# Kernel optimization log

Hardware: AMD Instinct MI355X
Metric: run time of the kernel (lower is better)

## Reference

```python
import jax, jax.numpy as jnp
import numpy as np
import itertools

N = 65536          # points
R = 1.0 / 16.0     # radius (forward uses 1/16)
K = 64             # max_num_neighbors in forward call
G = 16             # grid cells per axis (cell size == R)


def _radius_knn_edges(pts):
    """Grid-hashed radius search; per point keep nearest K within R (self-loop included),
    pad with self index so every point has exactly K edges (max-aggregation neutral)."""
    cells = np.minimum((pts / R).astype(np.int64), G - 1)
    cid = (cells[:, 0] * G + cells[:, 1]) * G + cells[:, 2]
    order = np.argsort(cid, kind='stable')
    sorted_cid = cid[order]
    counts = np.bincount(cid, minlength=G ** 3)
    starts = np.concatenate([[0], np.cumsum(counts)[:-1]])
    M = int(counts.max())
    cand = -np.ones((G ** 3, M), dtype=np.int64)
    slot = np.arange(N) - starts[sorted_cid]
    cand[sorted_cid, slot] = order
    offs = np.array(list(itertools.product([-1, 0, 1], repeat=3)))
    nbr = np.empty((N, K), dtype=np.int64)
    chunk = 4096
    for s in range(0, N, chunk):
        e = min(s + chunk, N)
        c = cells[s:e]
        nc = c[:, None, :] + offs[None]                      # [B,27,3]
        valid_c = np.all((nc >= 0) & (nc < G), axis=-1)      # [B,27]
        ncid = (nc[..., 0] * G + nc[..., 1]) * G + nc[..., 2]
        ncid = np.where(valid_c, ncid, 0)
        cd = cand[ncid]                                      # [B,27,M]
        cd = np.where(np.broadcast_to(valid_c[..., None], cd.shape), cd, -1)
        cd = cd.reshape(e - s, -1)                           # [B,27M]
        p = pts[np.maximum(cd, 0)]
        d = np.linalg.norm(p - pts[s:e, None, :], axis=-1)
        d = np.where((cd >= 0) & (d <= R), d, np.inf)
        sel = np.argsort(d, axis=1)[:, :K]
        row = np.arange(e - s)[:, None]
        picked = cd[row, sel]
        ok = np.isfinite(d[row, sel])
        nbr[s:e] = np.where(ok, picked, np.arange(s, e)[:, None])
    out_index = np.repeat(np.arange(N, dtype=np.int64), K)
    in_index = nbr.reshape(-1)
    return out_index, in_index


def setup_inputs() -> dict:
    key = jax.random.key(0)
    ks = jax.random.split(key, 16)
    pos = jax.random.uniform(ks[0], (N, 3), dtype=jnp.float32)
    rgb = jax.random.uniform(ks[1], (N, 3), dtype=jnp.float32)
    batch = jnp.zeros((N,), dtype=jnp.int64)
    oi, ii = _radius_knn_edges(np.asarray(pos, dtype=np.float64))
    out_index = jnp.asarray(oi)
    in_index = jnp.asarray(ii)

    def lin_w(k, fi, fo):
        return jax.random.normal(k, (fi, fo), dtype=jnp.float32) / np.sqrt(fi).astype(np.float32)

    def lin_b(k, fo):
        return 0.01 * jax.random.normal(k, (fo,), dtype=jnp.float32)

    return {
        'pos': pos, 'rgb': rgb, 'batch': batch,
        'out_index': out_index, 'in_index': in_index,
        'w1a': lin_w(ks[2], 6, 8),   'b1a': lin_b(ks[3], 8),
        'w1b': lin_w(ks[4], 8, 8),   'b1b': lin_b(ks[5], 8),
        'w2a': lin_w(ks[6], 11, 16), 'b2a': lin_b(ks[7], 16),
        'w2b': lin_w(ks[8], 16, 16), 'b2b': lin_b(ks[9], 16),
        'w3a': lin_w(ks[10], 19, 32), 'b3a': lin_b(ks[11], 32),
        'w3b': lin_w(ks[12], 32, 32), 'b3b': lin_b(ks[13], 32),
    }


def _point_conv(x, pos, out_index, in_index, wa, ba, wb, bb):
    # gather neighbor features + relative position, local MLP, max-scatter, output linear
    dpos = pos[in_index] - pos[out_index]                      # [E,3]
    msg = jnp.concatenate([x[in_index], dpos], axis=-1)        # [E,c_in+3]
    h = jax.nn.celu(msg @ wa + ba)                             # [E,c_mid]
    agg = jax.ops.segment_max(h, out_index, num_segments=pos.shape[0],
                              indices_are_sorted=True)         # [N,c_mid]
    return agg @ wb + bb                                       # [N,c_out]


def reference(pos, rgb, batch, out_index, in_index,
              w1a, b1a, w1b, b1b, w2a, b2a, w2b, b2b, w3a, b3a, w3b, b3b):
    out = jax.nn.celu(_point_conv(pos, pos, out_index, in_index, w1a, b1a, w1b, b1b))
    out = jax.nn.celu(_point_conv(out, pos, out_index, in_index, w2a, b2a, w2b, b2b))
    out = jax.nn.celu(_point_conv(out, pos, out_index, in_index, w3a, b3a, w3b, b3b))
    return (pos, out, batch)
```

## Files before the change

kernel.cpp:

```cpp
#include <hip/hip_runtime.h>
#include <hip/hip_fp16.h>
#include <math.h>


#define NPTS 65536
#define KNBR 64
#define GRES 16
#define NCELL 4096

__device__ __forceinline__ float celu1(float x) {
    return x > 0.0f ? x : (__expf(x) - 1.0f);
}

__device__ __forceinline__ unsigned pkmax(unsigned a, unsigned b) {
    unsigned d;
    asm("v_pk_max_f16 %0, %1, %2" : "=v"(d) : "v"(a), "v"(b));
    return d;
}

__device__ __forceinline__ unsigned pack2(float a, float b) {
    __half2 h = __floats2half2_rn(a, b);
    return *(unsigned*)&h;
}

__device__ __forceinline__ int cell_of(float p0, float p1, float p2) {
    int cx = min((int)(p0 * 16.0f), 15);
    int cy = min((int)(p1 * 16.0f), 15);
    int cz = min((int)(p2 * 16.0f), 15);
    return (cx * GRES + cy) * GRES + cz;
}


__global__ __launch_bounds__(256) void k_zero(int* __restrict__ buf) {
    buf[blockIdx.x * 256 + threadIdx.x] = 0;
}

__global__ __launch_bounds__(256) void k_hist(
    const float* __restrict__ pos, int* __restrict__ counts)
{
    int t = blockIdx.x * 256 + threadIdx.x;
    if (t >= NPTS) return;
    int cid = cell_of(pos[3 * t], pos[3 * t + 1], pos[3 * t + 2]);
    atomicAdd(&counts[cid], 1);
}

__global__ void k_scan(const int* __restrict__ counts, int* __restrict__ starts) {
    int lane = threadIdx.x;
    const int4* cp = (const int4*)counts;
    int4 c[16];
#pragma unroll
    for (int k = 0; k < 16; ++k) c[k] = cp[lane * 16 + k];
    int T = 0;
#pragma unroll
    for (int k = 0; k < 16; ++k) T += c[k].x + c[k].y + c[k].z + c[k].w;
    int inc = T;
#pragma unroll
    for (int d = 1; d < 64; d <<= 1) {
        int u = __shfl_up(inc, d, 64);
        if (lane >= d) inc += u;
    }
    int run = inc - T;
    int4* sp = (int4*)starts;
#pragma unroll
    for (int k = 0; k < 16; ++k) {
        int4 v = c[k], o;
        o.x = run; run += v.x;
        o.y = run; run += v.y;
        o.z = run; run += v.z;
        o.w = run; run += v.w;
        sp[lane * 16 + k] = o;
    }
}

__global__ __launch_bounds__(256) void k_slot(
    const float* __restrict__ pos,
    const int* __restrict__ starts, int* __restrict__ cursor,
    int* __restrict__ slot_of, int* __restrict__ perm,
    float* __restrict__ pos_s,
    const float* __restrict__ w1a, const float* __restrict__ b1a,
    __half* __restrict__ q1,
    float* __restrict__ dout, int out_size)
{
    int t = blockIdx.x * 256 + threadIdx.x;
    if (t >= NPTS) return;
    float p0 = pos[3 * t + 0];
    float p1 = pos[3 * t + 1];
    float p2 = pos[3 * t + 2];
    dout[3 * t + 0] = p0;
    dout[3 * t + 1] = p1;
    dout[3 * t + 2] = p2;
    for (int j = 35 * NPTS + t; j < out_size; j += NPTS)
        dout[j] = 0.0f;

    int cid = cell_of(p0, p1, p2);
    int s = starts[cid] + atomicAdd(&cursor[cid], 1);
    slot_of[t] = s;
    perm[s] = t;
    pos_s[3 * s + 0] = p0;
    pos_s[3 * s + 1] = p1;
    pos_s[3 * s + 2] = p2;

    float q[8];
#pragma unroll
    for (int c = 0; c < 8; ++c) {
        float a = b1a[c];
        a = fmaf(p0, w1a[0 * 8 + c] + w1a[3 * 8 + c], a);
        a = fmaf(p1, w1a[1 * 8 + c] + w1a[4 * 8 + c], a);
        a = fmaf(p2, w1a[2 * 8 + c] + w1a[5 * 8 + c], a);
        q[c] = a;
    }
    uint4 pk;
    pk.x = pack2(q[0], q[1]);
    pk.y = pack2(q[2], q[3]);
    pk.z = pack2(q[4], q[5]);
    pk.w = pack2(q[6], q[7]);
    *(uint4*)(q1 + 8 * s) = pk;
}

__global__ __launch_bounds__(256) void k_remap(
    const int* __restrict__ idx,
    const int* __restrict__ perm,
    const int* __restrict__ slot_of,
    int* __restrict__ idxs)
{
    int w = (blockIdx.x * 256 + threadIdx.x) >> 6;
    int k = threadIdx.x & 63;
    int src = perm[w];
    int j = idx[src * 64 + k];
    idxs[w * 64 + k] = slot_of[j];
}

template <int FH>
__global__ __launch_bounds__(256) void k_edge(
    const __half* __restrict__ q,
    const int* __restrict__ idx,
    __half* __restrict__ m)
{
    constexpr int SL  = FH / 8;
    constexpr int EG  = 16 / SL;
    constexpr int EPG = 64 / EG;

    int wave = (blockIdx.x * 256 + threadIdx.x) >> 6;
    int l  = threadIdx.x & 63;
    int pl = l >> 4;
    int u  = l & 15;
    int c  = u % SL;
    int g  = u / SL;
    int p  = wave * 4 + pl;

    const uint4* ip = (const uint4*)(idx + p * KNBR + g * EPG);
    uint4 iv[EPG / 4];
#pragma unroll
    for (int k = 0; k < EPG / 4; ++k) iv[k] = ip[k];

    unsigned ax = 0xFC00FC00u, ay = 0xFC00FC00u, az = 0xFC00FC00u, aw = 0xFC00FC00u;
#pragma unroll
    for (int k = 0; k < EPG / 4; ++k) {
        int j0 = (int)iv[k].x, j1 = (int)iv[k].y, j2 = (int)iv[k].z, j3 = (int)iv[k].w;
        uint4 v0 = *(const uint4*)(q + j0 * FH + c * 8);
        uint4 v1 = *(const uint4*)(q + j1 * FH + c * 8);
        uint4 v2 = *(const uint4*)(q + j2 * FH + c * 8);
        uint4 v3 = *(const uint4*)(q + j3 * FH + c * 8);
        ax = pkmax(ax, v0.x); ay = pkmax(ay, v0.y); az = pkmax(az, v0.z); aw = pkmax(aw, v0.w);
        ax = pkmax(ax, v1.x); ay = pkmax(ay, v1.y); az = pkmax(az, v1.z); aw = pkmax(aw, v1.w);
        ax = pkmax(ax, v2.x); ay = pkmax(ay, v2.y); az = pkmax(az, v2.z); aw = pkmax(aw, v2.w);
        ax = pkmax(ax, v3.x); ay = pkmax(ay, v3.y); az = pkmax(az, v3.z); aw = pkmax(aw, v3.w);
    }
#pragma unroll
    for (int st = SL; st < 16; st <<= 1) {
        ax = pkmax(ax, (unsigned)__shfl_xor((int)ax, st, 64));
        ay = pkmax(ay, (unsigned)__shfl_xor((int)ay, st, 64));
        az = pkmax(az, (unsigned)__shfl_xor((int)az, st, 64));
        aw = pkmax(aw, (unsigned)__shfl_xor((int)aw, st, 64));
    }
    if (g == 0) {
        uint4 r; r.x = ax; r.y = ay; r.z = az; r.w = aw;
        *(uint4*)(m + p * FH + c * 8) = r;
    }
}

template <int FH, int FOUT, int FHN, bool WRITEX>
__global__ __launch_bounds__(256) void k_finish(
    const __half* __restrict__ m,
    const float* __restrict__ pos_s,
    const float* __restrict__ wap,
    const float* __restrict__ wb,
    const float* __restrict__ bb,
    const float* __restrict__ wan,
    const float* __restrict__ ban,
    const int* __restrict__ perm,
    float* __restrict__ xout,
    __half* __restrict__ qnext)
{
    int t = blockIdx.x * 256 + threadIdx.x;
    float p0 = pos_s[3 * t + 0];
    float p1 = pos_s[3 * t + 1];
    float p2 = pos_s[3 * t + 2];

    float h[FH];
    const uint4* mr = (const uint4*)(m + t * FH);
#pragma unroll
    for (int l = 0; l < FH / 8; ++l) {
        uint4 v = mr[l];
        unsigned w4[4] = {v.x, v.y, v.z, v.w};
#pragma unroll
        for (int k = 0; k < 4; ++k) {
            float2 f = __half22float2(*(__half2*)&w4[k]);
            h[l * 8 + k * 2 + 0] = f.x;
            h[l * 8 + k * 2 + 1] = f.y;
        }
    }
#pragma unroll
    for (int c = 0; c < FH; ++c) {
        float g = p0 * wap[c] + p1 * wap[FH + c] + p2 * wap[2 * FH + c];
        h[c] = celu1(h[c] - g);
    }
    float x[FOUT];
#pragma unroll
    for (int c2 = 0; c2 < FOUT; ++c2) {
        float a = bb[c2];
#pragma unroll
        for (int c = 0; c < FH; ++c)
            a = fmaf(h[c], wb[c * FOUT + c2], a);
        x[c2] = celu1(a);
    }
    if constexpr (WRITEX) {
        int orig = perm[t];
        float4* xo = (float4*)(xout + (long long)orig * FOUT);
#pragma unroll
        for (int c4 = 0; c4 < FOUT / 4; ++c4)
            xo[c4] = make_float4(x[4 * c4 + 0], x[4 * c4 + 1], x[4 * c4 + 2], x[4 * c4 + 3]);
    }
    if constexpr (FHN > 0) {
        float qn[FHN];
#pragma unroll
        for (int cn = 0; cn < FHN; ++cn) {
            float a = ban[cn];
#pragma unroll
            for (int c2 = 0; c2 < FOUT; ++c2)
                a = fmaf(x[c2], wan[c2 * FHN + cn], a);
            a = fmaf(p0, wan[(FOUT + 0) * FHN + cn], a);
            a = fmaf(p1, wan[(FOUT + 1) * FHN + cn], a);
            a = fmaf(p2, wan[(FOUT + 2) * FHN + cn], a);
            qn[cn] = a;
        }
        uint4* qo = (uint4*)(qnext + t * FHN);
#pragma unroll
        for (int l = 0; l < FHN / 8; ++l) {
            uint4 pk;
            pk.x = pack2(qn[l * 8 + 0], qn[l * 8 + 1]);
            pk.y = pack2(qn[l * 8 + 2], qn[l * 8 + 3]);
            pk.z = pack2(qn[l * 8 + 4], qn[l * 8 + 5]);
            pk.w = pack2(qn[l * 8 + 6], qn[l * 8 + 7]);
            qo[l] = pk;
        }
    }
}

extern "C" void kernel_launch(void* const* d_in, const int* in_sizes, int n_in,
                              void* d_out, int out_size, void* d_ws, size_t ws_size,
                              hipStream_t stream) {
    const float* pos = (const float*)d_in[0];
    const int* idx = (const int*)d_in[4];
    const float* w1a = (const float*)d_in[5];
    const float* b1a = (const float*)d_in[6];
    const float* w1b = (const float*)d_in[7];
    const float* b1b = (const float*)d_in[8];
    const float* w2a = (const float*)d_in[9];
    const float* b2a = (const float*)d_in[10];
    const float* w2b = (const float*)d_in[11];
    const float* b2b = (const float*)d_in[12];
    const float* w3a = (const float*)d_in[13];
    const float* b3a = (const float*)d_in[14];
    const float* w3b = (const float*)d_in[15];
    const float* b3b = (const float*)d_in[16];
    float* out = (float*)d_out;

    char* ws = (char*)d_ws;
    int*    idxs    = (int*)ws;
    __half* A       = (__half*)(ws + (16u << 20));
    __half* B       = (__half*)(ws + (20u << 20));
    float*  pos_s   = (float*)(ws + (24u << 20));
    int*    slot_of = (int*)(ws + (25u << 20));
    int*    perm    = (int*)(ws + (25u << 20) + (256u << 10));
    int*    counts  = (int*)(ws + (26u << 20));
    int*    cursor  = counts + NCELL;
    int*    starts  = cursor + NCELL;

    k_zero<<<2 * NCELL / 256, 256, 0, stream>>>(counts);
    k_hist<<<NPTS / 256, 256, 0, stream>>>(pos, counts);
    k_scan<<<1, 64, 0, stream>>>(counts, starts);
    k_slot<<<NPTS / 256, 256, 0, stream>>>(pos, starts, cursor, slot_of, perm,
                                           pos_s, w1a, b1a, A, out, out_size);
    k_remap<<<NPTS / 4, 256, 0, stream>>>(idx, perm, slot_of, idxs);

    k_edge<8><<<NPTS / 16, 256, 0, stream>>>(A, idxs, B);
    k_finish<8, 8, 16, false><<<NPTS / 256, 256, 0, stream>>>(
        B, pos_s, w1a + 3 * 8, w1b, b1b, w2a, b2a, perm, nullptr, A);
    k_edge<16><<<NPTS / 16, 256, 0, stream>>>(A, idxs, B);
    k_finish<16, 16, 32, false><<<NPTS / 256, 256, 0, stream>>>(
        B, pos_s, w2a + 8 * 16, w2b, b2b, w3a, b3a, perm, nullptr, A);
    k_edge<32><<<NPTS / 16, 256, 0, stream>>>(A, idxs, B);
    k_finish<32, 32, 0, true><<<NPTS / 256, 256, 0, stream>>>(
        B, pos_s, w3a + 16 * 32, w3b, b3b, nullptr, nullptr, perm, out + 3 * NPTS, nullptr);
}
```

Baseline: 199.3 us.

## Process one grid cell per block with neighbor-cell rows staged in LDS

Each layer now runs one block per grid cell and stages the feature rows of the 27 surrounding cells in shared memory. Edge indices are remapped once into 16-bit local slots within that 27-cell window. The edge max-aggregation and the per-point MLP finish are fused into one kernel through an LDS buffer, which removes the intermediate global round trip and repeated scattered global gathers. The cost is load imbalance across cells of different occupancy and a global fallback path when the neighborhood exceeds the LDS capacity. It also assumes each cell holds at most 128 points.

```diff
diff --git a/kernel.cpp b/kernel.cpp
--- a/kernel.cpp
+++ b/kernel.cpp
@@ -28,6 +28,35 @@
     int cy = min((int)(p1 * 16.0f), 15);
     int cz = min((int)(p2 * 16.0f), 15);
     return (cx * GRES + cy) * GRES + cz;
+}
+
+__device__ __forceinline__ void build_desc(
+    int cid, const int* __restrict__ starts, const int* __restrict__ counts,
+    int* s_start, int* s_pfx)
+{
+    if (threadIdx.x < 64) {
+        int lane = threadIdx.x;
+        int cnt = 0, st = 0;
+        if (lane < 27) {
+            int cx = cid >> 8, cy = (cid >> 4) & 15, cz = cid & 15;
+            int dx = lane / 9 - 1, dy = (lane / 3) % 3 - 1, dz = lane % 3 - 1;
+            int nx = cx + dx, ny = cy + dy, nz = cz + dz;
+            bool ok = ((unsigned)nx < 16u) && ((unsigned)ny < 16u) && ((unsigned)nz < 16u);
+            if (ok) {
+                int nc = (((nx << 4) | ny) << 4) | nz;
+                cnt = counts[nc];
+                st  = starts[nc];
+            }
+        }
+        int inc = cnt;
+#pragma unroll
+        for (int d = 1; d < 32; d <<= 1) {
+            int u = __shfl_up(inc, d, 64);
+            if (lane >= d) inc += u;
+        }
+        if (lane < 27) { s_start[lane] = st; s_pfx[lane] = inc - cnt; }
+        if (lane == 26) s_pfx[27] = inc;
+    }
 }
 
 
@@ -76,6 +105,7 @@
     const float* __restrict__ pos,
     const int* __restrict__ starts, int* __restrict__ cursor,
     int* __restrict__ slot_of, int* __restrict__ perm,
+    unsigned short* __restrict__ cell16,
     float* __restrict__ pos_s,
     const float* __restrict__ w1a, const float* __restrict__ b1a,
     __half* __restrict__ q1,
@@ -96,6 +126,7 @@
     int s = starts[cid] + atomicAdd(&cursor[cid], 1);
     slot_of[t] = s;
     perm[s] = t;
+    cell16[s] = (unsigned short)cid;
     pos_s[3 * s + 0] = p0;
     pos_s[3 * s + 1] = p1;
     pos_s[3 * s + 2] = p2;
@@ -121,138 +152,179 @@
     const int* __restrict__ idx,
     const int* __restrict__ perm,
     const int* __restrict__ slot_of,
-    int* __restrict__ idxs)
-{
-    int w = (blockIdx.x * 256 + threadIdx.x) >> 6;
-    int k = threadIdx.x & 63;
-    int src = perm[w];
-    int j = idx[src * 64 + k];
-    idxs[w * 64 + k] = slot_of[j];
-}
-
-template <int FH>
-__global__ __launch_bounds__(256) void k_edge(
+    const unsigned short* __restrict__ cell16,
+    const int* __restrict__ starts,
+    const int* __restrict__ counts,
+    unsigned short* __restrict__ es)
+{
+    __shared__ int s_start[27];
+    __shared__ int s_pfx[28];
+    int cid = blockIdx.x;
+    build_desc(cid, starts, counts, s_start, s_pfx);
+    __syncthreads();
+
+    int base = starts[cid];
+    int P = counts[cid];
+    int cx = cid >> 8, cy = (cid >> 4) & 15, cz = cid & 15;
+    int tasks = P * 64;
+    for (int task = threadIdx.x; task < tasks; task += 256) {
+        int p_s = base + (task >> 6);
+        int e = task & 63;
+        int orig = perm[p_s];
+        int j_orig = idx[orig * 64 + e];
+        int j_s = slot_of[j_orig];
+        int jc = cell16[j_s];
+        int r = ((jc >> 8) - cx + 1) * 9 + (((jc >> 4) & 15) - cy + 1) * 3 + ((jc & 15) - cz + 1);
+        int slot = s_pfx[r] + (j_s - s_start[r]);
+        es[p_s * 64 + e] = (unsigned short)slot;
+    }
+}
+
+template <int FH, int FOUT, int FHN, bool WRITEX, int SCAP>
+__global__ __launch_bounds__(256) void k_layer(
     const __half* __restrict__ q,
-    const int* __restrict__ idx,
-    __half* __restrict__ m)
-{
-    constexpr int SL  = FH / 8;
-    constexpr int EG  = 16 / SL;
-    constexpr int EPG = 64 / EG;
-
-    int wave = (blockIdx.x * 256 + threadIdx.x) >> 6;
-    int l  = threadIdx.x & 63;
-    int pl = l >> 4;
-    int u  = l & 15;
-    int c  = u % SL;
-    int g  = u / SL;
-    int p  = wave * 4 + pl;
-
-    const uint4* ip = (const uint4*)(idx + p * KNBR + g * EPG);
-    uint4 iv[EPG / 4];
-#pragma unroll
-    for (int k = 0; k < EPG / 4; ++k) iv[k] = ip[k];
-
-    unsigned ax = 0xFC00FC00u, ay = 0xFC00FC00u, az = 0xFC00FC00u, aw = 0xFC00FC00u;
-#pragma unroll
-    for (int k = 0; k < EPG / 4; ++k) {
-        int j0 = (int)iv[k].x, j1 = (int)iv[k].y, j2 = (int)iv[k].z, j3 = (int)iv[k].w;
-        uint4 v0 = *(const uint4*)(q + j0 * FH + c * 8);
-        uint4 v1 = *(const uint4*)(q + j1 * FH + c * 8);
-        uint4 v2 = *(const uint4*)(q + j2 * FH + c * 8);
-        uint4 v3 = *(const uint4*)(q + j3 * FH + c * 8);
-        ax = pkmax(ax, v0.x); ay = pkmax(ay, v0.y); az = pkmax(az, v0.z); aw = pkmax(aw, v0.w);
-        ax = pkmax(ax, v1.x); ay = pkmax(ay, v1.y); az = pkmax(az, v1.z); aw = pkmax(aw, v1.w);
-        ax = pkmax(ax, v2.x); ay = pkmax(ay, v2.y); az = pkmax(az, v2.z); aw = pkmax(aw, v2.w);
-        ax = pkmax(ax, v3.x); ay = pkmax(ay, v3.y); az = pkmax(az, v3.z); aw = pkmax(aw, v3.w);
-    }
-#pragma unroll
-    for (int st = SL; st < 16; st <<= 1) {
-        ax = pkmax(ax, (unsigned)__shfl_xor((int)ax, st, 64));
-        ay = pkmax(ay, (unsigned)__shfl_xor((int)ay, st, 64));
-        az = pkmax(az, (unsigned)__shfl_xor((int)az, st, 64));
-        aw = pkmax(aw, (unsigned)__shfl_xor((int)aw, st, 64));
-    }
-    if (g == 0) {
-        uint4 r; r.x = ax; r.y = ay; r.z = az; r.w = aw;
-        *(uint4*)(m + p * FH + c * 8) = r;
-    }
-}
-
-template <int FH, int FOUT, int FHN, bool WRITEX>
-__global__ __launch_bounds__(256) void k_finish(
-    const __half* __restrict__ m,
+    const unsigned short* __restrict__ es,
     const float* __restrict__ pos_s,
+    const int* __restrict__ starts,
+    const int* __restrict__ counts,
+    const int* __restrict__ perm,
     const float* __restrict__ wap,
     const float* __restrict__ wb,
     const float* __restrict__ bb,
     const float* __restrict__ wan,
     const float* __restrict__ ban,
-    const int* __restrict__ perm,
     float* __restrict__ xout,
     __half* __restrict__ qnext)
 {
-    int t = blockIdx.x * 256 + threadIdx.x;
-    float p0 = pos_s[3 * t + 0];
-    float p1 = pos_s[3 * t + 1];
-    float p2 = pos_s[3 * t + 2];
-
-    float h[FH];
-    const uint4* mr = (const uint4*)(m + t * FH);
-#pragma unroll
-    for (int l = 0; l < FH / 8; ++l) {
-        uint4 v = mr[l];
-        unsigned w4[4] = {v.x, v.y, v.z, v.w};
-#pragma unroll
-        for (int k = 0; k < 4; ++k) {
-            float2 f = __half22float2(*(__half2*)&w4[k]);
-            h[l * 8 + k * 2 + 0] = f.x;
-            h[l * 8 + k * 2 + 1] = f.y;
-        }
-    }
-#pragma unroll
-    for (int c = 0; c < FH; ++c) {
-        float g = p0 * wap[c] + p1 * wap[FH + c] + p2 * wap[2 * FH + c];
-        h[c] = celu1(h[c] - g);
-    }
-    float x[FOUT];
-#pragma unroll
-    for (int c2 = 0; c2 < FOUT; ++c2) {
-        float a = bb[c2];
-#pragma unroll
-        for (int c = 0; c < FH; ++c)
-            a = fmaf(h[c], wb[c * FOUT + c2], a);
-        x[c2] = celu1(a);
-    }
-    if constexpr (WRITEX) {
-        int orig = perm[t];
-        float4* xo = (float4*)(xout + (long long)orig * FOUT);
-#pragma unroll
-        for (int c4 = 0; c4 < FOUT / 4; ++c4)
-            xo[c4] = make_float4(x[4 * c4 + 0], x[4 * c4 + 1], x[4 * c4 + 2], x[4 * c4 + 3]);
-    }
-    if constexpr (FHN > 0) {
-        float qn[FHN];
-#pragma unroll
-        for (int cn = 0; cn < FHN; ++cn) {
-            float a = ban[cn];
-#pragma unroll
-            for (int c2 = 0; c2 < FOUT; ++c2)
-                a = fmaf(x[c2], wan[c2 * FHN + cn], a);
-            a = fmaf(p0, wan[(FOUT + 0) * FHN + cn], a);
-            a = fmaf(p1, wan[(FOUT + 1) * FHN + cn], a);
-            a = fmaf(p2, wan[(FOUT + 2) * FHN + cn], a);
-            qn[cn] = a;
-        }
-        uint4* qo = (uint4*)(qnext + t * FHN);
-#pragma unroll
-        for (int l = 0; l < FHN / 8; ++l) {
-            uint4 pk;
-            pk.x = pack2(qn[l * 8 + 0], qn[l * 8 + 1]);
-            pk.y = pack2(qn[l * 8 + 2], qn[l * 8 + 3]);
-            pk.z = pack2(qn[l * 8 + 4], qn[l * 8 + 5]);
-            pk.w = pack2(qn[l * 8 + 6], qn[l * 8 + 7]);
-            qo[l] = pk;
+    constexpr int SL  = FH / 8;
+    constexpr int EPP = 64 / SL;
+
+    __shared__ int s_start[27];
+    __shared__ int s_pfx[28];
+    __shared__ uint4 rows[SCAP * SL];
+    __shared__ uint4 m_lds[128 * SL];
+
+    int cid = blockIdx.x;
+    build_desc(cid, starts, counts, s_start, s_pfx);
+    __syncthreads();
+
+    int total = s_pfx[27];
+    int stot = min(total, SCAP);
+    for (int s = threadIdx.x; s < stot; s += 256) {
+        int r = 0;
+        while (s >= s_pfx[r + 1]) ++r;
+        int row_g = s_start[r] + (s - s_pfx[r]);
+        const uint4* src = (const uint4*)(q + row_g * FH);
+#pragma unroll
+        for (int k = 0; k < SL; ++k) rows[s * SL + k] = src[k];
+    }
+    __syncthreads();
+
+    int base = starts[cid];
+    int P = counts[cid];
+    int w = threadIdx.x >> 6;
+    int l = threadIdx.x & 63;
+    int c  = l % SL;
+    int ep = l / SL;
+
+    for (int pl = w; pl < P; pl += 4) {
+        int p = base + pl;
+        int sv[SL];
+#pragma unroll
+        for (int pass = 0; pass < SL; ++pass)
+            sv[pass] = es[p * 64 + pass * EPP + ep];
+        unsigned ax = 0xFC00FC00u, ay = 0xFC00FC00u, az = 0xFC00FC00u, aw = 0xFC00FC00u;
+#pragma unroll
+        for (int pass = 0; pass < SL; ++pass) {
+            int s = sv[pass];
+            uint4 v;
+            if (s < stot) {
+                v = rows[s * SL + c];
+            } else {
+                int r = 0;
+                while (s >= s_pfx[r + 1]) ++r;
+                int row_g = s_start[r] + (s - s_pfx[r]);
+                v = *(const uint4*)(q + row_g * FH + c * 8);
+            }
+            ax = pkmax(ax, v.x); ay = pkmax(ay, v.y);
+            az = pkmax(az, v.z); aw = pkmax(aw, v.w);
+        }
+#pragma unroll
+        for (int st = SL; st < 64; st <<= 1) {
+            ax = pkmax(ax, (unsigned)__shfl_xor((int)ax, st, 64));
+            ay = pkmax(ay, (unsigned)__shfl_xor((int)ay, st, 64));
+            az = pkmax(az, (unsigned)__shfl_xor((int)az, st, 64));
+            aw = pkmax(aw, (unsigned)__shfl_xor((int)aw, st, 64));
+        }
+        if (ep == 0) {
+            uint4 r4; r4.x = ax; r4.y = ay; r4.z = az; r4.w = aw;
+            m_lds[pl * SL + c] = r4;
+        }
+    }
+    __syncthreads();
+
+    for (int lt = threadIdx.x; lt < P; lt += 256) {
+        int p = base + lt;
+        float p0 = pos_s[3 * p + 0];
+        float p1 = pos_s[3 * p + 1];
+        float p2 = pos_s[3 * p + 2];
+
+        float h[FH];
+#pragma unroll
+        for (int k = 0; k < SL; ++k) {
+            uint4 vv = m_lds[lt * SL + k];
+            unsigned w4[4] = {vv.x, vv.y, vv.z, vv.w};
+#pragma unroll
+            for (int kk = 0; kk < 4; ++kk) {
+                float2 f = __half22float2(*(__half2*)&w4[kk]);
+                h[k * 8 + kk * 2 + 0] = f.x;
+                h[k * 8 + kk * 2 + 1] = f.y;
+            }
+        }
+#pragma unroll
+        for (int ch = 0; ch < FH; ++ch) {
+            float gg = p0 * wap[ch] + p1 * wap[FH + ch] + p2 * wap[2 * FH + ch];
+            h[ch] = celu1(h[ch] - gg);
+        }
+        float x[FOUT];
+#pragma unroll
+        for (int c2 = 0; c2 < FOUT; ++c2) {
+            float a = bb[c2];
+#pragma unroll
+            for (int ch = 0; ch < FH; ++ch)
+                a = fmaf(h[ch], wb[ch * FOUT + c2], a);
+            x[c2] = celu1(a);
+        }
+        if constexpr (WRITEX) {
+            int orig = perm[p];
+            float4* xo = (float4*)(xout + (long long)orig * FOUT);
+#pragma unroll
+            for (int c4 = 0; c4 < FOUT / 4; ++c4)
+                xo[c4] = make_float4(x[4 * c4 + 0], x[4 * c4 + 1], x[4 * c4 + 2], x[4 * c4 + 3]);
+        }
+        if constexpr (FHN > 0) {
+            float qn[FHN];
+#pragma unroll
+            for (int cn = 0; cn < FHN; ++cn) {
+                float a = ban[cn];
+#pragma unroll
+                for (int c2 = 0; c2 < FOUT; ++c2)
+                    a = fmaf(x[c2], wan[c2 * FHN + cn], a);
+                a = fmaf(p0, wan[(FOUT + 0) * FHN + cn], a);
+                a = fmaf(p1, wan[(FOUT + 1) * FHN + cn], a);
+                a = fmaf(p2, wan[(FOUT + 2) * FHN + cn], a);
+                qn[cn] = a;
+            }
+            uint4* qo = (uint4*)(qnext + p * FHN);
+#pragma unroll
+            for (int k = 0; k < FHN / 8; ++k) {
+                uint4 pk;
+                pk.x = pack2(qn[k * 8 + 0], qn[k * 8 + 1]);
+                pk.y = pack2(qn[k * 8 + 2], qn[k * 8 + 3]);
+                pk.z = pack2(qn[k * 8 + 4], qn[k * 8 + 5]);
+                pk.w = pack2(qn[k * 8 + 6], qn[k * 8 + 7]);
+                qo[k] = pk;
+            }
         }
     }
 }
@@ -277,30 +349,32 @@
     float* out = (float*)d_out;
 
     char* ws = (char*)d_ws;
-    int*    idxs    = (int*)ws;
-    __half* A       = (__half*)(ws + (16u << 20));
-    __half* B       = (__half*)(ws + (20u << 20));
-    float*  pos_s   = (float*)(ws + (24u << 20));
-    int*    slot_of = (int*)(ws + (25u << 20));
-    int*    perm    = (int*)(ws + (25u << 20) + (256u << 10));
-    int*    counts  = (int*)(ws + (26u << 20));
-    int*    cursor  = counts + NCELL;
-    int*    starts  = cursor + NCELL;
+    unsigned short* es  = (unsigned short*)ws;
+    __half* q1          = (__half*)(ws + (8u << 20));
+    __half* q2          = (__half*)(ws + (9u << 20));
+    __half* q3          = (__half*)(ws + (11u << 20));
+    float*  pos_s       = (float*)(ws + (15u << 20));
+    int*    slot_of     = (int*)(ws + (16u << 20));
+    int*    perm        = (int*)(ws + (16u << 20) + (256u << 10));
+    unsigned short* c16 = (unsigned short*)(ws + (16u << 20) + (512u << 10));
+    int*    counts      = (int*)(ws + (17u << 20));
+    int*    cursor      = counts + NCELL;
+    int*    starts      = cursor + NCELL;
 
     k_zero<<<2 * NCELL / 256, 256, 0, stream>>>(counts);
     k_hist<<<NPTS / 256, 256, 0, stream>>>(pos, counts);
     k_scan<<<1, 64, 0, stream>>>(counts, starts);
     k_slot<<<NPTS / 256, 256, 0, stream>>>(pos, starts, cursor, slot_of, perm,
-                                           pos_s, w1a, b1a, A, out, out_size);
-    k_remap<<<NPTS / 4, 256, 0, stream>>>(idx, perm, slot_of, idxs);
-
-    k_edge<8><<<NPTS / 16, 256, 0, stream>>>(A, idxs, B);
-    k_finish<8, 8, 16, false><<<NPTS / 256, 256, 0, stream>>>(
-        B, pos_s, w1a + 3 * 8, w1b, b1b, w2a, b2a, perm, nullptr, A);
-    k_edge<16><<<NPTS / 16, 256, 0, stream>>>(A, idxs, B);
-    k_finish<16, 16, 32, false><<<NPTS / 256, 256, 0, stream>>>(
-        B, pos_s, w2a + 8 * 16, w2b, b2b, w3a, b3a, perm, nullptr, A);
-    k_edge<32><<<NPTS / 16, 256, 0, stream>>>(A, idxs, B);
-    k_finish<32, 32, 0, true><<<NPTS / 256, 256, 0, stream>>>(
-        B, pos_s, w3a + 16 * 32, w3b, b3b, nullptr, nullptr, perm, out + 3 * NPTS, nullptr);
-}
+                                           c16, pos_s, w1a, b1a, q1, out, out_size);
+    k_remap<<<NCELL, 256, 0, stream>>>(idx, perm, slot_of, c16, starts, counts, es);
+
+    k_layer<8, 8, 16, false, 1024><<<NCELL, 256, 0, stream>>>(
+        q1, es, pos_s, starts, counts, perm,
+        w1a + 3 * 8, w1b, b1b, w2a, b2a, nullptr, q2);
+    k_layer<16, 16, 32, false, 1024><<<NCELL, 256, 0, stream>>>(
+        q2, es, pos_s, starts, counts, perm,
+        w2a + 8 * 16, w2b, b2b, w3a, b3a, nullptr, q3);
+    k_layer<32, 32, 0, true, 640><<<NCELL, 256, 0, stream>>>(
+        q3, es, pos_s, starts, counts, perm,
+        w3a + 16 * 32, w3b, b3b, nullptr, nullptr, out + 3 * NPTS, nullptr);
+}
```

After: 468.2 us. +135.0%, slower.
